# Kernel optimization log

Measured on AMD Instinct MI355X. Metric: run time of the kernel, lower is better.

The kernel has to match this reference:

```python
import jax, jax.numpy as jnp
import numpy as np

EPS = 1e-6

def _elu_feature_map(x):
    # fast_transformers default feature map: elu(x) + 1 (always positive)
    return jax.nn.elu(x) + 1.0

def setup_inputs() -> dict:
    key = jax.random.key(0)
    ks = jax.random.split(key, 7)
    f, n, c, hid = 1024, 64, 256, 1024
    s = 1.0 / np.sqrt(c)
    return {
        "x": jax.random.normal(ks[0], (f, n, c), dtype=jnp.float32),
        "Wq": jax.random.normal(ks[1], (c, hid), dtype=jnp.float32) * s,
        "bq": jax.random.normal(ks[2], (hid,), dtype=jnp.float32) * 0.01,
        "Wk": jax.random.normal(ks[3], (c, hid), dtype=jnp.float32) * s,
        "bk": jax.random.normal(ks[4], (hid,), dtype=jnp.float32) * 0.01,
        "Wv": jax.random.normal(ks[5], (c, hid), dtype=jnp.float32) * s,
        "bv": jax.random.normal(ks[6], (hid,), dtype=jnp.float32) * 0.01,
    }

def reference(x, Wq, bq, Wk, bk, Wv, bv):
    heads = 8
    f, n, c = x.shape
    xt = jnp.transpose(x, (1, 0, 2))  # (n, f, c): joints as batch, frames as sequence
    q = xt @ Wq + bq  # (n, f, hid)
    k = xt @ Wk + bk
    v = xt @ Wv + bv
    hid = q.shape[-1]
    d = hid // heads
    q = q.reshape(n, f, heads, d)
    k = k.reshape(n, f, heads, d)
    v = v.reshape(n, f, heads, d)
    # Linear (kernelized) attention, non-causal (FullMask + full LengthMask)
    Q = _elu_feature_map(q)  # (n, f, h, d)
    K = _elu_feature_map(k)
    KV = jnp.einsum('nshd,nshm->nhmd', K, v)          # (n, h, d_v, d_k)
    Ksum = K.sum(axis=1)                               # (n, h, d_k)
    Z = 1.0 / (jnp.einsum('nlhd,nhd->nlh', Q, Ksum) + EPS)  # (n, f, h)
    out = jnp.einsum('nlhd,nhmd,nlh->nlhm', Q, KV, Z)  # (n, f, h, d_v)
    # faithful to rearrange('f n h c -> n f (h c)') applied to (n, f, h, d):
    # swaps first two axes -> output shape (f, n, h*d)
    out = jnp.transpose(out, (1, 0, 2, 3)).reshape(f, n, hid)
    return out
```

## Files before the change

kernel.cpp:

```cpp
#include <hip/hip_runtime.h>
#include <hip/hip_bf16.h>

#define F 1024
#define N 64
#define C 256
#define HID 1024
#define NH 8
#define D 128

using bf16x8 = __attribute__((ext_vector_type(8))) short;
using u16x8  = __attribute__((ext_vector_type(8))) unsigned short;
using u16x4  = __attribute__((ext_vector_type(4))) unsigned short;
using f32x4  = __attribute__((ext_vector_type(4))) float;

__device__ __forceinline__ unsigned short f2b(float f) {
    union { float f; unsigned u; } v; v.f = f;
    unsigned u = v.u;
    unsigned r = (u + 0x7fffu + ((u >> 16) & 1u)) >> 16;
    return (unsigned short)r;
}
__device__ __forceinline__ float b2f(unsigned short h) {
    union { unsigned u; float f; } v; v.u = ((unsigned)h) << 16;
    return v.f;
}

__device__ __forceinline__ void load_lds16(const unsigned short* g, unsigned short* l) {
    __builtin_amdgcn_global_load_lds(
        (const __attribute__((address_space(1))) void*)g,
        (__attribute__((address_space(3))) void*)l, 16, 0, 0);
}

__global__ void k_conv_x(const float* __restrict__ x, unsigned short* __restrict__ xt) {
    int row = blockIdx.x * 4 + (threadIdx.x >> 6);
    int lane = threadIdx.x & 63;
    int fi = row >> 6, ni = row & 63;
    float4 a = *(const float4*)(x + row * C + lane * 4);
    u16x4 o;
    o[0] = f2b(a.x); o[1] = f2b(a.y); o[2] = f2b(a.z); o[3] = f2b(a.w);
    *(u16x4*)(xt + (ni * F + fi) * C + lane * 4) = o;
}

__global__ void k_conv_w(const float* __restrict__ Wq, const float* __restrict__ Wk,
                         const float* __restrict__ Wv, unsigned short* __restrict__ Wt) {
    int w = blockIdx.z;
    const float* W = (w == 0) ? Wq : ((w == 1) ? Wk : Wv);
    unsigned short* O = Wt + w * (HID * C);
    int n0 = blockIdx.x * 64, k0 = blockIdx.y * 64;
    __shared__ float t[64][65];
    int tx = threadIdx.x & 63, ty = threadIdx.x >> 6;
#pragma unroll
    for (int i = 0; i < 16; i++) {
        int kl = ty + i * 4;
        t[kl][tx] = W[(k0 + kl) * HID + n0 + tx];
    }
    __syncthreads();
#pragma unroll
    for (int i = 0; i < 16; i++) {
        int nl = ty + i * 4;
        O[(n0 + nl) * C + k0 + tx] = f2b(t[tx][nl]);
    }
}

#define CT_PITCH 136
__global__ __launch_bounds__(256, 2) void k_qkv(
    const unsigned short* __restrict__ xt, const unsigned short* __restrict__ Wt,
    const float* __restrict__ bq, const float* __restrict__ bk, const float* __restrict__ bv,
    unsigned short* __restrict__ Q, unsigned short* __restrict__ Kt,
    unsigned short* __restrict__ Vt) {
    __shared__ unsigned short smem[128 * CT_PITCH];
    unsigned short* Xs = smem;
    unsigned short* Ws = smem + 4096;
    unsigned short* Ct = smem;

    const int mt = blockIdx.x;
    const int ni = mt >> 3, fi0 = (mt & 7) << 7;
    const int u = blockIdx.y;
    const int out_id = u >> 3, h = u & 7;
    const int tid = threadIdx.x, lane = tid & 63, w = tid >> 6;
    const int quad = lane >> 4, l15 = lane & 15;
    const int wm = w >> 1, wn = w & 1;

    const unsigned short* Ag = xt + (ni * F + fi0) * C;
    const unsigned short* Bg = Wt + out_id * (HID * C) + (h * D) * C;

    const int srow = lane >> 2;
    const int scol = (lane & 3) * 8;

    const unsigned short* As_f = (out_id == 0) ? Xs : Ws;
    const unsigned short* Bs_f = (out_id == 0) ? Ws : Xs;

    f32x4 acc[4][4];
#pragma unroll
    for (int i = 0; i < 4; i++)
#pragma unroll
        for (int j = 0; j < 4; j++) acc[i][j] = (f32x4)0.f;

#pragma unroll
    for (int ks = 0; ks < 8; ks++) {
        const int kof = ks * 32;
        const unsigned short* ga = Ag + (w * 32 + srow) * C + kof + scol;
        const unsigned short* gb = Bg + (w * 32 + srow) * C + kof + scol;
        load_lds16(ga,            Xs + (w * 32) * 32);
        load_lds16(ga + 16 * C,   Xs + (w * 32 + 16) * 32);
        load_lds16(gb,            Ws + (w * 32) * 32);
        load_lds16(gb + 16 * C,   Ws + (w * 32 + 16) * 32);
        __syncthreads();

        bf16x8 af[4], bfr[4];
#pragma unroll
        for (int mb = 0; mb < 4; mb++)
            af[mb] = *(const bf16x8*)(As_f + (wm * 64 + mb * 16 + l15) * 32 + quad * 8);
#pragma unroll
        for (int nb = 0; nb < 4; nb++)
            bfr[nb] = *(const bf16x8*)(Bs_f + (wn * 64 + nb * 16 + l15) * 32 + quad * 8);
#pragma unroll
        for (int mb = 0; mb < 4; mb++)
#pragma unroll
            for (int nb = 0; nb < 4; nb++)
                acc[mb][nb] = __builtin_amdgcn_mfma_f32_16x16x32_bf16(
                    af[mb], bfr[nb], acc[mb][nb], 0, 0, 0);
        __syncthreads();
    }

    const float* bias = ((out_id == 0) ? bq : ((out_id == 1) ? bk : bv)) + h * D;

    if (out_id == 0) {
        float bcol[4];
#pragma unroll
        for (int nb = 0; nb < 4; nb++) bcol[nb] = bias[wn * 64 + nb * 16 + l15];
#pragma unroll
        for (int mb = 0; mb < 4; mb++)
#pragma unroll
            for (int r = 0; r < 4; r++) {
                int row = wm * 64 + mb * 16 + quad * 4 + r;
#pragma unroll
                for (int nb = 0; nb < 4; nb++) {
                    int col = wn * 64 + nb * 16 + l15;
                    float v = acc[mb][nb][r] + bcol[nb];
                    v = (v > 0.f) ? (v + 1.f) : __expf(v);
                    Ct[row * CT_PITCH + col] = f2b(v);
                }
            }
    } else {
        const bool isk = (out_id == 1);
#pragma unroll
        for (int mb = 0; mb < 4; mb++)
#pragma unroll
            for (int r = 0; r < 4; r++) {
                int row = wm * 64 + mb * 16 + quad * 4 + r;
                float bb = bias[row];
#pragma unroll
                for (int nb = 0; nb < 4; nb++) {
                    int col = wn * 64 + nb * 16 + l15;
                    float v = acc[mb][nb][r] + bb;
                    if (isk) v = (v > 0.f) ? (v + 1.f) : __expf(v);
                    Ct[row * CT_PITCH + col] = f2b(v);
                }
            }
    }
    __syncthreads();

    if (out_id == 0) {
        unsigned short* Op = Q + (ni * NH + h) * (F * D) + fi0 * D;
#pragma unroll
        for (int chunk = 0; chunk < 8; chunk++) {
            int idx = chunk * 256 + tid;
            int row = idx >> 4, col = (idx & 15) * 8;
            u16x8 v = *(const u16x8*)(Ct + row * CT_PITCH + col);
            *(u16x8*)(Op + row * D + col) = v;
        }
    } else {
        unsigned short* Op = ((out_id == 1) ? Kt : Vt) + (ni * NH + h) * (D * F) + fi0;
#pragma unroll
        for (int chunk = 0; chunk < 8; chunk++) {
            int idx = chunk * 256 + tid;
            int row = idx >> 4, col = (idx & 15) * 8;
            u16x8 v = *(const u16x8*)(Ct + row * CT_PITCH + col);
            *(u16x8*)(Op + row * F + col) = v;
        }
    }
}

__global__ __launch_bounds__(256, 2) void k_kv(
    const unsigned short* __restrict__ Kt, const unsigned short* __restrict__ Vt,
    unsigned short* __restrict__ KV, float* __restrict__ Ksum) {
    __shared__ float sred[256];
    const int b = blockIdx.x;
    const unsigned short* Kp = Kt + b * (D * F);
    const unsigned short* Vp = Vt + b * (D * F);
    const int tid = threadIdx.x, lane = tid & 63, w = tid >> 6;
    const int quad = lane >> 4, l15 = lane & 15;

    {
        int d = tid >> 1, half = tid & 1;
        const unsigned short* row = Kp + d * F + half * 512;
        float s = 0.f;
        for (int i = 0; i < 512; i += 8) {
            u16x8 v = *(const u16x8*)(row + i);
#pragma unroll
            for (int j = 0; j < 8; j++) s += b2f(v[j]);
        }
        sred[tid] = s;
        __syncthreads();
        if (tid < 128) Ksum[b * D + tid] = sred[2 * tid] + sred[2 * tid + 1];
    }

    f32x4 acc[2][8];
#pragma unroll
    for (int a = 0; a < 2; a++)
#pragma unroll
        for (int c = 0; c < 8; c++) acc[a][c] = (f32x4)0.f;

    for (int s0 = 0; s0 < F; s0 += 32) {
        bf16x8 af[2], bfr[8];
#pragma unroll
        for (int mb = 0; mb < 2; mb++) {
            int m = w * 32 + mb * 16 + l15;
            af[mb] = *(const bf16x8*)(Vp + m * F + s0 + quad * 8);
        }
#pragma unroll
        for (int nb = 0; nb < 8; nb++) {
            int d = nb * 16 + l15;
            bfr[nb] = *(const bf16x8*)(Kp + d * F + s0 + quad * 8);
        }
#pragma unroll
        for (int mb = 0; mb < 2; mb++)
#pragma unroll
            for (int nb = 0; nb < 8; nb++)
                acc[mb][nb] = __builtin_amdgcn_mfma_f32_16x16x32_bf16(
                    af[mb], bfr[nb], acc[mb][nb], 0, 0, 0);
    }
    unsigned short* KVp = KV + b * (D * D);
#pragma unroll
    for (int mb = 0; mb < 2; mb++)
#pragma unroll
        for (int r = 0; r < 4; r++) {
            int m = w * 32 + mb * 16 + quad * 4 + r;
#pragma unroll
            for (int nb = 0; nb < 8; nb++) {
                int d = nb * 16 + l15;
                KVp[m * D + d] = f2b(acc[mb][nb][r]);
            }
        }
}

__global__ __launch_bounds__(256, 2) void k_out(
    const unsigned short* __restrict__ Q, const unsigned short* __restrict__ KV,
    const float* __restrict__ Ksum, float* __restrict__ out) {
    __shared__ float Kss[D];
    __shared__ float Zs[128];
    const int b = blockIdx.x, lt = blockIdx.y;
    const int ni = b >> 3, h = b & 7;
    const int l0 = lt * 128;
    const unsigned short* Qp = Q + b * (F * D) + l0 * D;
    const unsigned short* KVp = KV + b * (D * D);
    const int tid = threadIdx.x, lane = tid & 63, w = tid >> 6;
    const int quad = lane >> 4, l15 = lane & 15;
    const int wm = w >> 1, wn = w & 1;

    if (tid < 128) Kss[tid] = Ksum[b * D + tid];
    __syncthreads();
    if (tid < 128) {
        const unsigned short* qr = Qp + tid * D;
        float s = 0.f;
#pragma unroll
        for (int i = 0; i < D; i += 8) {
            u16x8 v = *(const u16x8*)(qr + i);
#pragma unroll
            for (int j = 0; j < 8; j++) s += b2f(v[j]) * Kss[i + j];
        }
        Zs[tid] = 1.f / (s + 1e-6f);
    }
    __syncthreads();

    f32x4 acc[4][4];
#pragma unroll
    for (int a = 0; a < 4; a++)
#pragma unroll
        for (int c = 0; c < 4; c++) acc[a][c] = (f32x4)0.f;

#pragma unroll
    for (int k0 = 0; k0 < D; k0 += 32) {
        bf16x8 af[4], bfr[4];
#pragma unroll
        for (int mb = 0; mb < 4; mb++) {
            int m = wm * 64 + mb * 16 + l15;
            af[mb] = *(const bf16x8*)(KVp + m * D + k0 + quad * 8);
        }
#pragma unroll
        for (int nb = 0; nb < 4; nb++) {
            int l = wn * 64 + nb * 16 + l15;
            bfr[nb] = *(const bf16x8*)(Qp + l * D + k0 + quad * 8);
        }
#pragma unroll
        for (int mb = 0; mb < 4; mb++)
#pragma unroll
            for (int nb = 0; nb < 4; nb++)
                acc[mb][nb] = __builtin_amdgcn_mfma_f32_16x16x32_bf16(
                    af[mb], bfr[nb], acc[mb][nb], 0, 0, 0);
    }

#pragma unroll
    for (int nb = 0; nb < 4; nb++) {
        int l = wn * 64 + nb * 16 + l15;
        float z = Zs[l];
        float* op = out + ((l0 + l) * N + ni) * HID + h * D;
#pragma unroll
        for (int mb = 0; mb < 4; mb++) {
            int m0 = wm * 64 + mb * 16 + quad * 4;
            float4 vv;
            vv.x = acc[mb][nb][0] * z;
            vv.y = acc[mb][nb][1] * z;
            vv.z = acc[mb][nb][2] * z;
            vv.w = acc[mb][nb][3] * z;
            *(float4*)(op + m0) = vv;
        }
    }
}

extern "C" void kernel_launch(void* const* d_in, const int* in_sizes, int n_in,
                              void* d_out, int out_size, void* d_ws, size_t ws_size,
                              hipStream_t stream) {
    const float* x  = (const float*)d_in[0];
    const float* Wq = (const float*)d_in[1];
    const float* bq = (const float*)d_in[2];
    const float* Wk = (const float*)d_in[3];
    const float* bk = (const float*)d_in[4];
    const float* Wv = (const float*)d_in[5];
    const float* bv = (const float*)d_in[6];
    float* out = (float*)d_out;
    char* ws = (char*)d_ws;

    unsigned short* xt   = (unsigned short*)(ws);
    unsigned short* Wt   = (unsigned short*)(ws + 33554432);
    unsigned short* Qb   = (unsigned short*)(ws + 35127296);
    unsigned short* Ktb  = (unsigned short*)(ws + 169345024);
    unsigned short* Vtb  = (unsigned short*)(ws + 303562752);
    unsigned short* KVb  = (unsigned short*)(ws + 437780480);
    float*          Ksum = (float*)(ws + 454557696);

    k_conv_x<<<16384, 256, 0, stream>>>(x, xt);
    k_conv_w<<<dim3(16, 4, 3), 256, 0, stream>>>(Wq, Wk, Wv, Wt);
    k_qkv<<<dim3(512, 24), 256, 0, stream>>>(xt, Wt, bq, bk, bv, Qb, Ktb, Vtb);
    k_kv<<<512, 256, 0, stream>>>(Ktb, Vtb, KVb, Ksum);
    k_out<<<dim3(512, 8), 256, 0, stream>>>(Qb, KVb, Ksum, out);
}
```

Before: 709.0 us.

## Fuse QKV projection into KV-reduction and output kernels, dropping Q/K/V intermediates

```diff
diff --git a/kernel.cpp b/kernel.cpp
--- a/kernel.cpp
+++ b/kernel.cpp
@@ -61,58 +61,190 @@
     }
 }
 
-#define CT_PITCH 136
-__global__ __launch_bounds__(256, 2) void k_qkv(
+__global__ __launch_bounds__(256, 2) void k_kv_fused(
     const unsigned short* __restrict__ xt, const unsigned short* __restrict__ Wt,
-    const float* __restrict__ bq, const float* __restrict__ bk, const float* __restrict__ bv,
-    unsigned short* __restrict__ Q, unsigned short* __restrict__ Kt,
-    unsigned short* __restrict__ Vt) {
-    __shared__ unsigned short smem[128 * CT_PITCH];
-    unsigned short* Xs = smem;
-    unsigned short* Ws = smem + 4096;
-    unsigned short* Ct = smem;
-
-    const int mt = blockIdx.x;
-    const int ni = mt >> 3, fi0 = (mt & 7) << 7;
-    const int u = blockIdx.y;
-    const int out_id = u >> 3, h = u & 7;
+    const float* __restrict__ bk, const float* __restrict__ bv,
+    unsigned short* __restrict__ KV, float* __restrict__ Ksum) {
+    __shared__ unsigned short Ks[128 * 128];
+    __shared__ unsigned short Vs[128 * 128];
+    __shared__ unsigned short Sx[128 * 32];
+    __shared__ unsigned short Sw[128 * 32];
+
+    const int ni = blockIdx.x & 63, h = blockIdx.x >> 6;
+    const int b = ni * NH + h;
     const int tid = threadIdx.x, lane = tid & 63, w = tid >> 6;
     const int quad = lane >> 4, l15 = lane & 15;
     const int wm = w >> 1, wn = w & 1;
-
-    const unsigned short* Ag = xt + (ni * F + fi0) * C;
-    const unsigned short* Bg = Wt + out_id * (HID * C) + (h * D) * C;
-
-    const int srow = lane >> 2;
-    const int scol = (lane & 3) * 8;
-
-    const unsigned short* As_f = (out_id == 0) ? Xs : Ws;
-    const unsigned short* Bs_f = (out_id == 0) ? Ws : Xs;
+    const int srow = lane >> 2, scol = (lane & 3) * 8;
+
+    const unsigned short* xb  = xt + ni * (F * C);
+    const unsigned short* Wkp = Wt + (HID * C) + (h * D) * C;
+    const unsigned short* Wvp = Wt + 2 * (HID * C) + (h * D) * C;
+    const float* bkp = bk + h * D;
+    const float* bvp = bv + h * D;
+
+    f32x4 acc2[4][4];
+#pragma unroll
+    for (int i = 0; i < 4; i++)
+#pragma unroll
+        for (int j = 0; j < 4; j++) acc2[i][j] = (f32x4)0.f;
+    float ksacc = 0.f;
+    const int zd = tid >> 1, zh = tid & 1;
+
+#pragma unroll 1
+    for (int ft = 0; ft < 8; ft++) {
+        const unsigned short* xrow = xb + (ft * 128) * C;
+#pragma unroll 1
+        for (int pv = 0; pv < 2; pv++) {
+            const unsigned short* Wp = pv ? Wvp : Wkp;
+            f32x4 acc[4][4];
+#pragma unroll
+            for (int i = 0; i < 4; i++)
+#pragma unroll
+                for (int j = 0; j < 4; j++) acc[i][j] = (f32x4)0.f;
+#pragma unroll
+            for (int ks = 0; ks < 8; ks++) {
+                const int kof = ks * 32;
+                const unsigned short* ga = xrow + (w * 32 + srow) * C + kof + scol;
+                const unsigned short* gw = Wp + (w * 32 + srow) * C + kof + scol;
+                load_lds16(ga,          Sx + (w * 32) * 32);
+                load_lds16(ga + 16 * C, Sx + (w * 32 + 16) * 32);
+                load_lds16(gw,          Sw + (w * 32) * 32);
+                load_lds16(gw + 16 * C, Sw + (w * 32 + 16) * 32);
+                __syncthreads();
+                bf16x8 af[4], bfr[4];
+#pragma unroll
+                for (int mb = 0; mb < 4; mb++)
+                    af[mb] = *(const bf16x8*)(Sw + (wm * 64 + mb * 16 + l15) * 32 + quad * 8);
+#pragma unroll
+                for (int nb = 0; nb < 4; nb++)
+                    bfr[nb] = *(const bf16x8*)(Sx + (wn * 64 + nb * 16 + l15) * 32 + quad * 8);
+#pragma unroll
+                for (int mb = 0; mb < 4; mb++)
+#pragma unroll
+                    for (int nb = 0; nb < 4; nb++)
+                        acc[mb][nb] = __builtin_amdgcn_mfma_f32_16x16x32_bf16(
+                            af[mb], bfr[nb], acc[mb][nb], 0, 0, 0);
+                __syncthreads();
+            }
+            const float* bias = pv ? bvp : bkp;
+            unsigned short* T = pv ? Vs : Ks;
+#pragma unroll
+            for (int mb = 0; mb < 4; mb++)
+#pragma unroll
+                for (int r = 0; r < 4; r++) {
+                    int dd = wm * 64 + mb * 16 + quad * 4 + r;
+                    float bb = bias[dd];
+                    char* rowp = (char*)T + dd * 256;
+                    int sw = (dd & 7) << 4;
+#pragma unroll
+                    for (int nb = 0; nb < 4; nb++) {
+                        int fi = wn * 64 + nb * 16 + l15;
+                        float v = acc[mb][nb][r] + bb;
+                        if (!pv) v = (v > 0.f) ? (v + 1.f) : __expf(v);
+                        *(unsigned short*)(rowp + ((fi * 2) ^ sw)) = f2b(v);
+                    }
+                }
+        }
+        __syncthreads();
+#pragma unroll
+        for (int k0 = 0; k0 < 128; k0 += 32) {
+            bf16x8 af[4], bfr[4];
+#pragma unroll
+            for (int mb = 0; mb < 4; mb++) {
+                int m = wm * 64 + mb * 16 + l15;
+                af[mb] = *(const bf16x8*)((const char*)Vs + m * 256 +
+                                          (((k0 + quad * 8) * 2) ^ ((m & 7) << 4)));
+            }
+#pragma unroll
+            for (int nb = 0; nb < 4; nb++) {
+                int d = wn * 64 + nb * 16 + l15;
+                bfr[nb] = *(const bf16x8*)((const char*)Ks + d * 256 +
+                                           (((k0 + quad * 8) * 2) ^ ((d & 7) << 4)));
+            }
+#pragma unroll
+            for (int mb = 0; mb < 4; mb++)
+#pragma unroll
+                for (int nb = 0; nb < 4; nb++)
+                    acc2[mb][nb] = __builtin_amdgcn_mfma_f32_16x16x32_bf16(
+                        af[mb], bfr[nb], acc2[mb][nb], 0, 0, 0);
+        }
+        {
+            const char* kr = (const char*)Ks + zd * 256;
+            int sw = (zd & 7) << 4;
+#pragma unroll
+            for (int c = 0; c < 8; c++) {
+                u16x8 v = *(const u16x8*)(kr + (((zh * 8 + c) * 16) ^ sw));
+#pragma unroll
+                for (int j = 0; j < 8; j++) ksacc += b2f(v[j]);
+            }
+        }
+    }
+
+    unsigned short* KVp = KV + b * (D * D);
+#pragma unroll
+    for (int mb = 0; mb < 4; mb++)
+#pragma unroll
+        for (int r = 0; r < 4; r++) {
+            int m = wm * 64 + mb * 16 + quad * 4 + r;
+#pragma unroll
+            for (int nb = 0; nb < 4; nb++) {
+                int d = wn * 64 + nb * 16 + l15;
+                KVp[m * D + d] = f2b(acc2[mb][nb][r]);
+            }
+        }
+    __syncthreads();
+    float* sred = (float*)Sx;
+    sred[tid] = ksacc;
+    __syncthreads();
+    if (tid < 128) Ksum[b * D + tid] = sred[2 * tid] + sred[2 * tid + 1];
+}
+
+__global__ __launch_bounds__(256, 3) void k_out_fused(
+    const unsigned short* __restrict__ xt, const unsigned short* __restrict__ Wt,
+    const float* __restrict__ bq, const unsigned short* __restrict__ KV,
+    const float* __restrict__ Ksum, float* __restrict__ out) {
+    __shared__ unsigned short Qs[128 * 128];
+    __shared__ unsigned short Sx[128 * 32];
+    __shared__ unsigned short Sw[128 * 32];
+    __shared__ float Kss[128];
+    __shared__ float Zs[128];
+
+    const int ni = blockIdx.x & 63, h = blockIdx.x >> 6;
+    const int b = ni * NH + h;
+    const int l0 = blockIdx.y * 128;
+    const int tid = threadIdx.x, lane = tid & 63, w = tid >> 6;
+    const int quad = lane >> 4, l15 = lane & 15;
+    const int wm = w >> 1, wn = w & 1;
+    const int srow = lane >> 2, scol = (lane & 3) * 8;
+
+    if (tid < 128) Kss[tid] = Ksum[b * D + tid];
+
+    const unsigned short* xrow = xt + (ni * F + l0) * C;
+    const unsigned short* Wqp = Wt + (h * D) * C;
 
     f32x4 acc[4][4];
 #pragma unroll
     for (int i = 0; i < 4; i++)
 #pragma unroll
         for (int j = 0; j < 4; j++) acc[i][j] = (f32x4)0.f;
-
 #pragma unroll
     for (int ks = 0; ks < 8; ks++) {
         const int kof = ks * 32;
-        const unsigned short* ga = Ag + (w * 32 + srow) * C + kof + scol;
-        const unsigned short* gb = Bg + (w * 32 + srow) * C + kof + scol;
-        load_lds16(ga,            Xs + (w * 32) * 32);
-        load_lds16(ga + 16 * C,   Xs + (w * 32 + 16) * 32);
-        load_lds16(gb,            Ws + (w * 32) * 32);
-        load_lds16(gb + 16 * C,   Ws + (w * 32 + 16) * 32);
+        const unsigned short* ga = xrow + (w * 32 + srow) * C + kof + scol;
+        const unsigned short* gw = Wqp + (w * 32 + srow) * C + kof + scol;
+        load_lds16(ga,          Sx + (w * 32) * 32);
+        load_lds16(ga + 16 * C, Sx + (w * 32 + 16) * 32);
+        load_lds16(gw,          Sw + (w * 32) * 32);
+        load_lds16(gw + 16 * C, Sw + (w * 32 + 16) * 32);
         __syncthreads();
-
         bf16x8 af[4], bfr[4];
 #pragma unroll
         for (int mb = 0; mb < 4; mb++)
-            af[mb] = *(const bf16x8*)(As_f + (wm * 64 + mb * 16 + l15) * 32 + quad * 8);
+            af[mb] = *(const bf16x8*)(Sx + (wm * 64 + mb * 16 + l15) * 32 + quad * 8);
 #pragma unroll
         for (int nb = 0; nb < 4; nb++)
-            bfr[nb] = *(const bf16x8*)(Bs_f + (wn * 64 + nb * 16 + l15) * 32 + quad * 8);
+            bfr[nb] = *(const bf16x8*)(Sw + (wn * 64 + nb * 16 + l15) * 32 + quad * 8);
 #pragma unroll
         for (int mb = 0; mb < 4; mb++)
 #pragma unroll
@@ -121,166 +253,48 @@
                     af[mb], bfr[nb], acc[mb][nb], 0, 0, 0);
         __syncthreads();
     }
-
-    const float* bias = ((out_id == 0) ? bq : ((out_id == 1) ? bk : bv)) + h * D;
-
-    if (out_id == 0) {
+    {
         float bcol[4];
 #pragma unroll
-        for (int nb = 0; nb < 4; nb++) bcol[nb] = bias[wn * 64 + nb * 16 + l15];
+        for (int nb = 0; nb < 4; nb++) bcol[nb] = bq[h * D + wn * 64 + nb * 16 + l15];
 #pragma unroll
         for (int mb = 0; mb < 4; mb++)
 #pragma unroll
             for (int r = 0; r < 4; r++) {
-                int row = wm * 64 + mb * 16 + quad * 4 + r;
+                int fi = wm * 64 + mb * 16 + quad * 4 + r;
+                char* rowp = (char*)Qs + fi * 256;
+                int sw = (fi & 7) << 4;
 #pragma unroll
                 for (int nb = 0; nb < 4; nb++) {
-                    int col = wn * 64 + nb * 16 + l15;
+                    int dd = wn * 64 + nb * 16 + l15;
                     float v = acc[mb][nb][r] + bcol[nb];
                     v = (v > 0.f) ? (v + 1.f) : __expf(v);
-                    Ct[row * CT_PITCH + col] = f2b(v);
+                    *(unsigned short*)(rowp + ((dd * 2) ^ sw)) = f2b(v);
                 }
             }
-    } else {
-        const bool isk = (out_id == 1);
-#pragma unroll
-        for (int mb = 0; mb < 4; mb++)
-#pragma unroll
-            for (int r = 0; r < 4; r++) {
-                int row = wm * 64 + mb * 16 + quad * 4 + r;
-                float bb = bias[row];
-#pragma unroll
-                for (int nb = 0; nb < 4; nb++) {
-                    int col = wn * 64 + nb * 16 + l15;
-                    float v = acc[mb][nb][r] + bb;
-                    if (isk) v = (v > 0.f) ? (v + 1.f) : __expf(v);
-                    Ct[row * CT_PITCH + col] = f2b(v);
-                }
-            }
-    }
-    __syncthreads();
-
-    if (out_id == 0) {
-        unsigned short* Op = Q + (ni * NH + h) * (F * D) + fi0 * D;
-#pragma unroll
-        for (int chunk = 0; chunk < 8; chunk++) {
-            int idx = chunk * 256 + tid;
-            int row = idx >> 4, col = (idx & 15) * 8;
-            u16x8 v = *(const u16x8*)(Ct + row * CT_PITCH + col);
-            *(u16x8*)(Op + row * D + col) = v;
-        }
-    } else {
-        unsigned short* Op = ((out_id == 1) ? Kt : Vt) + (ni * NH + h) * (D * F) + fi0;
-#pragma unroll
-        for (int chunk = 0; chunk < 8; chunk++) {
-            int idx = chunk * 256 + tid;
-            int row = idx >> 4, col = (idx & 15) * 8;
-            u16x8 v = *(const u16x8*)(Ct + row * CT_PITCH + col);
-            *(u16x8*)(Op + row * F + col) = v;
-        }
-    }
-}
-
-__global__ __launch_bounds__(256, 2) void k_kv(
-    const unsigned short* __restrict__ Kt, const unsigned short* __restrict__ Vt,
-    unsigned short* __restrict__ KV, float* __restrict__ Ksum) {
-    __shared__ float sred[256];
-    const int b = blockIdx.x;
-    const unsigned short* Kp = Kt + b * (D * F);
-    const unsigned short* Vp = Vt + b * (D * F);
-    const int tid = threadIdx.x, lane = tid & 63, w = tid >> 6;
-    const int quad = lane >> 4, l15 = lane & 15;
-
-    {
-        int d = tid >> 1, half = tid & 1;
-        const unsigned short* row = Kp + d * F + half * 512;
+    }
+    __syncthreads();
+    if (tid < 128) {
+        const char* qr = (const char*)Qs + tid * 256;
+        int sw = (tid & 7) << 4;
         float s = 0.f;
-        for (int i = 0; i < 512; i += 8) {
-            u16x8 v = *(const u16x8*)(row + i);
-#pragma unroll
-            for (int j = 0; j < 8; j++) s += b2f(v[j]);
-        }
-        sred[tid] = s;
-        __syncthreads();
-        if (tid < 128) Ksum[b * D + tid] = sred[2 * tid] + sred[2 * tid + 1];
-    }
-
-    f32x4 acc[2][8];
-#pragma unroll
-    for (int a = 0; a < 2; a++)
-#pragma unroll
-        for (int c = 0; c < 8; c++) acc[a][c] = (f32x4)0.f;
-
-    for (int s0 = 0; s0 < F; s0 += 32) {
-        bf16x8 af[2], bfr[8];
-#pragma unroll
-        for (int mb = 0; mb < 2; mb++) {
-            int m = w * 32 + mb * 16 + l15;
-            af[mb] = *(const bf16x8*)(Vp + m * F + s0 + quad * 8);
-        }
-#pragma unroll
-        for (int nb = 0; nb < 8; nb++) {
-            int d = nb * 16 + l15;
-            bfr[nb] = *(const bf16x8*)(Kp + d * F + s0 + quad * 8);
-        }
-#pragma unroll
-        for (int mb = 0; mb < 2; mb++)
-#pragma unroll
-            for (int nb = 0; nb < 8; nb++)
-                acc[mb][nb] = __builtin_amdgcn_mfma_f32_16x16x32_bf16(
-                    af[mb], bfr[nb], acc[mb][nb], 0, 0, 0);
-    }
-    unsigned short* KVp = KV + b * (D * D);
-#pragma unroll
-    for (int mb = 0; mb < 2; mb++)
-#pragma unroll
-        for (int r = 0; r < 4; r++) {
-            int m = w * 32 + mb * 16 + quad * 4 + r;
-#pragma unroll
-            for (int nb = 0; nb < 8; nb++) {
-                int d = nb * 16 + l15;
-                KVp[m * D + d] = f2b(acc[mb][nb][r]);
-            }
-        }
-}
-
-__global__ __launch_bounds__(256, 2) void k_out(
-    const unsigned short* __restrict__ Q, const unsigned short* __restrict__ KV,
-    const float* __restrict__ Ksum, float* __restrict__ out) {
-    __shared__ float Kss[D];
-    __shared__ float Zs[128];
-    const int b = blockIdx.x, lt = blockIdx.y;
-    const int ni = b >> 3, h = b & 7;
-    const int l0 = lt * 128;
-    const unsigned short* Qp = Q + b * (F * D) + l0 * D;
+#pragma unroll
+        for (int c = 0; c < 16; c++) {
+            u16x8 v = *(const u16x8*)(qr + ((c * 16) ^ sw));
+#pragma unroll
+            for (int j = 0; j < 8; j++) s += b2f(v[j]) * Kss[c * 8 + j];
+        }
+        Zs[tid] = 1.f / (s + 1e-6f);
+    }
+    __syncthreads();
     const unsigned short* KVp = KV + b * (D * D);
-    const int tid = threadIdx.x, lane = tid & 63, w = tid >> 6;
-    const int quad = lane >> 4, l15 = lane & 15;
-    const int wm = w >> 1, wn = w & 1;
-
-    if (tid < 128) Kss[tid] = Ksum[b * D + tid];
-    __syncthreads();
-    if (tid < 128) {
-        const unsigned short* qr = Qp + tid * D;
-        float s = 0.f;
-#pragma unroll
-        for (int i = 0; i < D; i += 8) {
-            u16x8 v = *(const u16x8*)(qr + i);
-#pragma unroll
-            for (int j = 0; j < 8; j++) s += b2f(v[j]) * Kss[i + j];
-        }
-        Zs[tid] = 1.f / (s + 1e-6f);
-    }
-    __syncthreads();
-
-    f32x4 acc[4][4];
-#pragma unroll
-    for (int a = 0; a < 4; a++)
-#pragma unroll
-        for (int c = 0; c < 4; c++) acc[a][c] = (f32x4)0.f;
-
-#pragma unroll
-    for (int k0 = 0; k0 < D; k0 += 32) {
+    f32x4 o4[4][4];
+#pragma unroll
+    for (int i = 0; i < 4; i++)
+#pragma unroll
+        for (int j = 0; j < 4; j++) o4[i][j] = (f32x4)0.f;
+#pragma unroll
+    for (int k0 = 0; k0 < 128; k0 += 32) {
         bf16x8 af[4], bfr[4];
 #pragma unroll
         for (int mb = 0; mb < 4; mb++) {
@@ -290,16 +304,16 @@
 #pragma unroll
         for (int nb = 0; nb < 4; nb++) {
             int l = wn * 64 + nb * 16 + l15;
-            bfr[nb] = *(const bf16x8*)(Qp + l * D + k0 + quad * 8);
+            bfr[nb] = *(const bf16x8*)((const char*)Qs + l * 256 +
+                                       (((k0 + quad * 8) * 2) ^ ((l & 7) << 4)));
         }
 #pragma unroll
         for (int mb = 0; mb < 4; mb++)
 #pragma unroll
             for (int nb = 0; nb < 4; nb++)
-                acc[mb][nb] = __builtin_amdgcn_mfma_f32_16x16x32_bf16(
-                    af[mb], bfr[nb], acc[mb][nb], 0, 0, 0);
-    }
-
+                o4[mb][nb] = __builtin_amdgcn_mfma_f32_16x16x32_bf16(
+                    af[mb], bfr[nb], o4[mb][nb], 0, 0, 0);
+    }
 #pragma unroll
     for (int nb = 0; nb < 4; nb++) {
         int l = wn * 64 + nb * 16 + l15;
@@ -309,10 +323,10 @@
         for (int mb = 0; mb < 4; mb++) {
             int m0 = wm * 64 + mb * 16 + quad * 4;
             float4 vv;
-            vv.x = acc[mb][nb][0] * z;
-            vv.y = acc[mb][nb][1] * z;
-            vv.z = acc[mb][nb][2] * z;
-            vv.w = acc[mb][nb][3] * z;
+            vv.x = o4[mb][nb][0] * z;
+            vv.y = o4[mb][nb][1] * z;
+            vv.z = o4[mb][nb][2] * z;
+            vv.w = o4[mb][nb][3] * z;
             *(float4*)(op + m0) = vv;
         }
     }
@@ -333,15 +347,11 @@
 
     unsigned short* xt   = (unsigned short*)(ws);
     unsigned short* Wt   = (unsigned short*)(ws + 33554432);
-    unsigned short* Qb   = (unsigned short*)(ws + 35127296);
-    unsigned short* Ktb  = (unsigned short*)(ws + 169345024);
-    unsigned short* Vtb  = (unsigned short*)(ws + 303562752);
-    unsigned short* KVb  = (unsigned short*)(ws + 437780480);
-    float*          Ksum = (float*)(ws + 454557696);
+    unsigned short* KVb  = (unsigned short*)(ws + 35127296);
+    float*          Ksum = (float*)(ws + 51904512);
 
     k_conv_x<<<16384, 256, 0, stream>>>(x, xt);
     k_conv_w<<<dim3(16, 4, 3), 256, 0, stream>>>(Wq, Wk, Wv, Wt);
-    k_qkv<<<dim3(512, 24), 256, 0, stream>>>(xt, Wt, bq, bk, bv, Qb, Ktb, Vtb);
-    k_kv<<<512, 256, 0, stream>>>(Ktb, Vtb, KVb, Ksum);
-    k_out<<<dim3(512, 8), 256, 0, stream>>>(Qb, KVb, Ksum, out);
-}
+    k_kv_fused<<<512, 256, 0, stream>>>(xt, Wt, bk, bv, KVb, Ksum);
+    k_out_fused<<<dim3(512, 8), 256, 0, stream>>>(xt, Wt, bq, KVb, Ksum, out);
+}
```

Result: faster. 609.3 us (-14.1%).
